# Kernel tuning notes

Measured on AMD Instinct MI355X. Metric: run time of the kernel, lower is better.

Reference implementation:

```python
import jax, jax.numpy as jnp
import numpy as np

DS = 32   # self_obs_dim
DO = 32   # obstacle_obs_dim
D = DS + DO
H = 128   # obstacle_hidden_size
B = 512   # batch_size
A = 16    # num_adv_obs = 2 * num_oppo_obs


def _init_linear(key, fan_in, fan_out):
    kw, kb = jax.random.split(key)
    bound = 1.0 / np.sqrt(fan_in)
    w = jax.random.uniform(kw, (fan_in, fan_out), jnp.float32, -bound, bound)
    b = jax.random.uniform(kb, (fan_out,), jnp.float32, -bound, bound)
    return w, b


def setup_inputs() -> dict:
    key = jax.random.key(0)
    ks = jax.random.split(key, 10)
    obs = jax.random.normal(ks[0], (B, DS), jnp.float32)
    latent = jax.random.normal(ks[1], (B, A, DO), jnp.float32)
    hw1, hb1 = _init_linear(ks[2], D, H)
    hw2, hb2 = _init_linear(ks[3], H, D * H)
    vw1, vb1 = _init_linear(ks[4], H, H)
    vw2, vb2 = _init_linear(ks[5], H, H)
    aw1, ab1 = _init_linear(ks[6], 2 * H, H)
    aw2, ab2 = _init_linear(ks[7], H, H)
    aw3, ab3 = _init_linear(ks[8], H, 1)
    return {
        "obs": obs, "obs_intention_latent": latent,
        "hw1": hw1, "hb1": hb1, "hw2": hw2, "hb2": hb2,
        "vw1": vw1, "vb1": vb1, "vw2": vw2, "vb2": vb2,
        "aw1": aw1, "ab1": ab1, "aw2": aw2, "ab2": ab2,
        "aw3": aw3, "ab3": ab3,
        "num_adv_obs": A, "batch_size": B, "num_groups": 1,
    }


def reference(obs, obs_intention_latent, hw1, hb1, hw2, hb2,
              vw1, vb1, vw2, vb2, aw1, ab1, aw2, ab2, aw3, ab3,
              num_adv_obs, batch_size, num_groups):
    relu = jax.nn.relu
    # flatten opponents (batch-major, matches torch .reshape)
    obs_obstacles = obs_intention_latent.reshape(-1, DO)          # [N, DO]
    # torch .repeat(num_adv_obs, 1) tiles the batch dim
    self_rep = jnp.tile(obs[:, :DS], (num_adv_obs, 1))            # [N, DS]
    mlp_input = jnp.concatenate([self_rep, obs_obstacles], axis=1)  # [N, D]
    # hypernet: per-sample weight [N, D, H]
    h = relu(mlp_input @ hw1 + hb1)
    w = relu(h @ hw2 + hb2).reshape(-1, D, H)
    # per-sample vector-matrix product + tanh
    emb = jnp.tanh(jnp.einsum("nd,ndh->nh", mlp_input, w))        # [N, H]
    # neighbor value MLP
    vals = relu(relu(emb @ vw1 + vb1) @ vw2 + vb2)                # [N, H]
    # attention: concat with per-batch mean embedding
    emb_mean = jnp.mean(emb.reshape(batch_size, -1, H), axis=1)   # [B, H]
    mean_rep = jnp.tile(emb_mean, (num_adv_obs, 1))               # [N, H]
    att_in = jnp.concatenate([emb, mean_rep], axis=1)             # [N, 2H]
    scores = relu(relu(att_in @ aw1 + ab1) @ aw2 + ab2) @ aw3 + ab3  # [N, 1]
    att = jax.nn.softmax(scores.reshape(batch_size, -1), axis=1).reshape(-1, 1)
    weighted = (att * vals).reshape(batch_size, -1, H)
    return jnp.sum(weighted, axis=1)                              # [B, H]
```

## Files before the change

### kernel.cpp

```cpp
#include <hip/hip_runtime.h>
#include <hip/hip_bf16.h>
#include <math.h>

#define BATCH 512
#define NADV  16
#define NROWS (BATCH*NADV)
#define DS    32
#define DO    32
#define DIM   64
#define HID   128
#define WCOLS (DIM*HID)
#define LSTR  136
#define PACK_BLOCKS 276

typedef _Float16 half8 __attribute__((ext_vector_type(8)));
typedef float floatx4 __attribute__((ext_vector_type(4)));

__device__ inline void async_ld16(void* lds, const void* g) {
    __builtin_amdgcn_global_load_lds(
        (const __attribute__((address_space(1))) void*)g,
        (__attribute__((address_space(3))) void*)lds, 16, 0, 0);
}

__global__ __launch_bounds__(256)
void k_prep(const float* __restrict__ obs, const float* __restrict__ latent,
            const float* __restrict__ hw1, const float* __restrict__ hb1,
            const float* __restrict__ hw2, const float* __restrict__ vw1,
            const float* __restrict__ vw2, const float* __restrict__ aw1,
            const float* __restrict__ aw2,
            _Float16* __restrict__ hf,
            _Float16* __restrict__ w2p, _Float16* __restrict__ vw1p,
            _Float16* __restrict__ vw2p, _Float16* __restrict__ aw1p,
            _Float16* __restrict__ aw2p) {
    __shared__ __align__(16) float smem[32 * 132];
    int b = blockIdx.x;
    int tid = threadIdx.x;
    if (b < PACK_BLOCKS) {
        const float* src; _Float16* dst; int N, Kt, jb, kt;
        if (b < 256)      { src = hw2; dst = w2p;  N = WCOLS; Kt = 4; jb = b >> 2; kt = b & 3; }
        else if (b < 260) { src = vw1; dst = vw1p; N = HID;   Kt = 4; jb = 0; kt = b - 256; }
        else if (b < 264) { src = vw2; dst = vw2p; N = HID;   Kt = 4; jb = 0; kt = b - 260; }
        else if (b < 272) { src = aw1; dst = aw1p; N = HID;   Kt = 8; jb = 0; kt = b - 264; }
        else              { src = aw2; dst = aw2p; N = HID;   Kt = 4; jb = 0; kt = b - 272; }
        for (int i = tid; i < 32 * 32; i += 256) {
            int r = i >> 5, c4 = (i & 31) * 4;
            *(float4*)&smem[r * 132 + c4] =
                *(const float4*)(src + (size_t)(kt * 32 + r) * N + jb * 128 + c4);
        }
        __syncthreads();
        for (int i = tid; i < 8 * 64; i += 256) {
            int ctl = i >> 6, lane = i & 63;
            int ct = jb * 8 + ctl;
            int rbase = (lane >> 4) * 8, cc = ctl * 16 + (lane & 15);
            half8 v;
#pragma unroll
            for (int e = 0; e < 8; ++e) v[e] = (_Float16)smem[(rbase + e) * 132 + cc];
            *(half8*)(dst + ((size_t)ct * Kt + kt) * 512 + lane * 8) = v;
        }
    } else {
        int n0 = (b - PACK_BLOCKS) * 16;
        int wave = tid >> 6, lane = tid & 63, l15 = lane & 15, quad = lane >> 4;
        half8 af2[2];
        {
            int n = n0 + l15;
            const float* orow = obs + (size_t)(n & (BATCH - 1)) * DS + quad * 8;
            const float* lrow = latent + (size_t)n * DO + quad * 8;
            float4 a0 = *(const float4*)orow;
            float4 a1 = *(const float4*)(orow + 4);
            float4 c0 = *(const float4*)lrow;
            float4 c1 = *(const float4*)(lrow + 4);
            float a8[8] = {a0.x, a0.y, a0.z, a0.w, a1.x, a1.y, a1.z, a1.w};
            float c8[8] = {c0.x, c0.y, c0.z, c0.w, c1.x, c1.y, c1.z, c1.w};
#pragma unroll
            for (int e = 0; e < 8; ++e) {
                af2[0][e] = (_Float16)a8[e];
                af2[1][e] = (_Float16)c8[e];
            }
        }
#pragma unroll
        for (int cti = 0; cti < 2; ++cti) {
            int ct = wave * 2 + cti;
            float bb = hb1[ct * 16 + l15];
            floatx4 acc = {bb, bb, bb, bb};
#pragma unroll
            for (int ks = 0; ks < 2; ++ks) {
                const float* wsrc = hw1 + (size_t)(ks * 32 + quad * 8) * HID + ct * 16 + l15;
                half8 bf;
#pragma unroll
                for (int e = 0; e < 8; ++e) bf[e] = (_Float16)wsrc[e * HID];
                acc = __builtin_amdgcn_mfma_f32_16x16x32_f16(af2[ks], bf, acc, 0, 0, 0);
            }
#pragma unroll
            for (int reg = 0; reg < 4; ++reg)
                hf[(size_t)(n0 + quad * 4 + reg) * HID + ct * 16 + l15] =
                    (_Float16)fmaxf(acc[reg], 0.f);
        }
    }
}

__global__ __launch_bounds__(256, 2)
void k_hyper_mfma(const float* __restrict__ obs, const float* __restrict__ latent,
                  const _Float16* __restrict__ hf, const _Float16* __restrict__ w2p,
                  const float* __restrict__ hb2,
                  _Float16* __restrict__ embf, _Float16* __restrict__ emeanf) {
    __shared__ __align__(16) _Float16 Bs[8][4][512];
    __shared__ __align__(16) float xs_t[64][132];
    __shared__ float bias_s[64 * 16];
    int b  = blockIdx.x;
    int jt = b & 7;
    int rt = b >> 3;
    int n0 = rt * 128;
    int j0 = jt * 16;
    int tid = threadIdx.x;
    int wave = tid >> 6, lane = tid & 63;
    int l15 = lane & 15, quad = lane >> 4;

    for (int i = tid; i < 128 * 16; i += 256) {
        int r = i >> 4, c4 = (i & 15) * 4;
        float4 v;
        if (c4 < DS) v = *(const float4*)(obs + ((n0 + r) & (BATCH - 1)) * DS + c4);
        else         v = *(const float4*)(latent + (size_t)(n0 + r) * DO + (c4 - DS));
        xs_t[c4 + 0][r] = v.x;
        xs_t[c4 + 1][r] = v.y;
        xs_t[c4 + 2][r] = v.z;
        xs_t[c4 + 3][r] = v.w;
    }
    for (int i = tid; i < 64 * 16; i += 256)
        bias_s[i] = hb2[(i >> 4) * HID + j0 + (i & 15)];

    half8 af[2][4];
#pragma unroll
    for (int t = 0; t < 2; ++t) {
        const _Float16* arow = hf + (size_t)(n0 + wave * 32 + t * 16 + l15) * HID;
#pragma unroll
        for (int ks = 0; ks < 4; ++ks)
            af[t][ks] = *(const half8*)(arow + ks * 32 + quad * 8);
    }

    float emb_acc[2][4] = {{0.f, 0.f, 0.f, 0.f}, {0.f, 0.f, 0.f, 0.f}};

    for (int d8 = 0; d8 < 8; ++d8) {
#pragma unroll
        for (int s = 0; s < 2; ++s) {
            int dt = wave * 2 + s;
            int ct = (d8 * 8 + dt) * 8 + jt;
            const _Float16* src = w2p + (size_t)ct * 2048 + lane * 8;
            _Float16* dst = &Bs[dt][0][0];
#pragma unroll
            for (int kt = 0; kt < 4; ++kt)
                async_ld16(dst + kt * 512, src + kt * 512);
        }
        __syncthreads();

#pragma unroll
        for (int dd = 0; dd < 8; ++dd) {
            int d = d8 * 8 + dd;
            float bb = bias_s[d * 16 + l15];
            floatx4 acc0 = {bb, bb, bb, bb};
            floatx4 acc1 = {bb, bb, bb, bb};
#pragma unroll
            for (int ks = 0; ks < 4; ++ks) {
                half8 bfr = *(const half8*)&Bs[dd][ks][lane * 8];
                acc0 = __builtin_amdgcn_mfma_f32_16x16x32_f16(af[0][ks], bfr, acc0, 0, 0, 0);
                acc1 = __builtin_amdgcn_mfma_f32_16x16x32_f16(af[1][ks], bfr, acc1, 0, 0, 0);
            }
            floatx4 xv0 = *(const floatx4*)&xs_t[d][wave * 32 + quad * 4];
            floatx4 xv1 = *(const floatx4*)&xs_t[d][wave * 32 + 16 + quad * 4];
#pragma unroll
            for (int reg = 0; reg < 4; ++reg) {
                emb_acc[0][reg] = fmaf(xv0[reg], fmaxf(acc0[reg], 0.f), emb_acc[0][reg]);
                emb_acc[1][reg] = fmaf(xv1[reg], fmaxf(acc1[reg], 0.f), emb_acc[1][reg]);
            }
        }
        __syncthreads();
    }

#pragma unroll
    for (int t = 0; t < 2; ++t) {
        float e[4];
#pragma unroll
        for (int reg = 0; reg < 4; ++reg) {
            e[reg] = tanhf(emb_acc[t][reg]);
            embf[(size_t)(n0 + wave * 32 + t * 16 + quad * 4 + reg) * HID + j0 + l15] =
                (_Float16)e[reg];
        }
        float s = e[0] + e[1] + e[2] + e[3];
        s += __shfl_xor(s, 16, 64);
        s += __shfl_xor(s, 32, 64);
        if (quad == 0)
            emeanf[(size_t)(rt * 8 + wave * 2 + t) * HID + j0 + l15] =
                (_Float16)(s * (1.f / 16));
    }
}

__global__ __launch_bounds__(512, 4)
void k_tail(const _Float16* __restrict__ embf, const _Float16* __restrict__ emeanf,
            const _Float16* __restrict__ vw1p, const float* __restrict__ vb1,
            const _Float16* __restrict__ vw2p, const float* __restrict__ vb2,
            const _Float16* __restrict__ aw1p, const float* __restrict__ ab1,
            const _Float16* __restrict__ aw2p, const float* __restrict__ ab2,
            const float* __restrict__ aw3, const float* __restrict__ ab3,
            float* __restrict__ out) {
    __shared__ _Float16 embs[16][LSTR];
    __shared__ _Float16 means[16][LSTR];
    __shared__ _Float16 tAs[16][LSTR];
    __shared__ _Float16 tBs[16][LSTR];
    __shared__ float scr[16][32];
    __shared__ float satt[16];
    __shared__ float att[16];
    int g = blockIdx.x;
    int n0 = g * 16;
    int tid = threadIdx.x;
    int wave = tid >> 6, lane = tid & 63, l15 = lane & 15, quad = lane >> 4;
    int ct = wave;

    {
        int m = tid >> 8, r = (tid >> 4) & 15, c8 = (tid & 15) * 8;
        if (m == 0)
            *(half8*)&embs[r][c8] = *(const half8*)(embf + (size_t)(n0 + r) * HID + c8);
        else
            *(half8*)&means[r][c8] =
                *(const half8*)(emeanf + (size_t)((n0 & 511) + r) * HID + c8);
    }
    __syncthreads();

    half8 av[4], amean[4];
#pragma unroll
    for (int ks = 0; ks < 4; ++ks) {
        av[ks]    = *(const half8*)&embs[l15][ks * 32 + quad * 8];
        amean[ks] = *(const half8*)&means[l15][ks * 32 + quad * 8];
    }

    floatx4 acc;
    {
        float bb = vb1[ct * 16 + l15];
        acc = (floatx4){bb, bb, bb, bb};
    }
#pragma unroll
    for (int ks = 0; ks < 4; ++ks) {
        half8 bfr = *(const half8*)(vw1p + ((size_t)ct * 4 + ks) * 512 + lane * 8);
        acc = __builtin_amdgcn_mfma_f32_16x16x32_f16(av[ks], bfr, acc, 0, 0, 0);
    }
#pragma unroll
    for (int reg = 0; reg < 4; ++reg)
        tAs[quad * 4 + reg][ct * 16 + l15] = (_Float16)fmaxf(acc[reg], 0.f);
    __syncthreads();

    half8 at[4];
#pragma unroll
    for (int ks = 0; ks < 4; ++ks)
        at[ks] = *(const half8*)&tAs[l15][ks * 32 + quad * 8];

    floatx4 vacc;
    {
        float bb = vb2[ct * 16 + l15];
        vacc = (floatx4){bb, bb, bb, bb};
    }
#pragma unroll
    for (int ks = 0; ks < 4; ++ks) {
        half8 bfr = *(const half8*)(vw2p + ((size_t)ct * 4 + ks) * 512 + lane * 8);
        vacc = __builtin_amdgcn_mfma_f32_16x16x32_f16(at[ks], bfr, vacc, 0, 0, 0);
    }

    floatx4 aacc;
    {
        float bb = ab1[ct * 16 + l15];
        aacc = (floatx4){bb, bb, bb, bb};
    }
#pragma unroll
    for (int ks = 0; ks < 8; ++ks) {
        half8 bfr = *(const half8*)(aw1p + ((size_t)ct * 8 + ks) * 512 + lane * 8);
        half8 a = (ks < 4) ? av[ks] : amean[ks - 4];
        aacc = __builtin_amdgcn_mfma_f32_16x16x32_f16(a, bfr, aacc, 0, 0, 0);
    }
#pragma unroll
    for (int reg = 0; reg < 4; ++reg)
        tBs[quad * 4 + reg][ct * 16 + l15] = (_Float16)fmaxf(aacc[reg], 0.f);
    __syncthreads();

    half8 aa[4];
#pragma unroll
    for (int ks = 0; ks < 4; ++ks)
        aa[ks] = *(const half8*)&tBs[l15][ks * 32 + quad * 8];

    floatx4 a2acc;
    {
        float bb = ab2[ct * 16 + l15];
        a2acc = (floatx4){bb, bb, bb, bb};
    }
#pragma unroll
    for (int ks = 0; ks < 4; ++ks) {
        half8 bfr = *(const half8*)(aw2p + ((size_t)ct * 4 + ks) * 512 + lane * 8);
        a2acc = __builtin_amdgcn_mfma_f32_16x16x32_f16(aa[ks], bfr, a2acc, 0, 0, 0);
    }
    __syncthreads();
#pragma unroll
    for (int reg = 0; reg < 4; ++reg)
        tAs[quad * 4 + reg][ct * 16 + l15] = (_Float16)fmaxf(a2acc[reg], 0.f);
    __syncthreads();

    {
        int r = tid >> 5, ch = tid & 31;
        float p = 0.f;
#pragma unroll
        for (int k = 0; k < 4; ++k)
            p += (float)tAs[r][ch * 4 + k] * aw3[ch * 4 + k];
        scr[r][ch] = p;
    }
    __syncthreads();
    if (tid < 16) {
        float s = ab3[0];
#pragma unroll
        for (int ch = 0; ch < 32; ++ch) s += scr[tid][ch];
        satt[tid] = s;
    }
    __syncthreads();
    if (tid < 16) {
        float m = -1e30f;
#pragma unroll
        for (int a = 0; a < 16; ++a) m = fmaxf(m, satt[a]);
        float S = 0.f;
#pragma unroll
        for (int a = 0; a < 16; ++a) S += expf(satt[a] - m);
        att[tid] = expf(satt[tid] - m) / S;
    }
    __syncthreads();

    {
        float p = 0.f;
#pragma unroll
        for (int reg = 0; reg < 4; ++reg)
            p += att[quad * 4 + reg] * fmaxf(vacc[reg], 0.f);
        p += __shfl_xor(p, 16, 64);
        p += __shfl_xor(p, 32, 64);
        if (quad == 0) out[(size_t)g * HID + ct * 16 + l15] = p;
    }
}

extern "C" void kernel_launch(void* const* d_in, const int* in_sizes, int n_in,
                              void* d_out, int out_size, void* d_ws, size_t ws_size,
                              hipStream_t stream) {
    const float* obs = (const float*)d_in[0];
    const float* lat = (const float*)d_in[1];
    const float* hw1 = (const float*)d_in[2];
    const float* hb1 = (const float*)d_in[3];
    const float* hw2 = (const float*)d_in[4];
    const float* hb2 = (const float*)d_in[5];
    const float* vw1 = (const float*)d_in[6];
    const float* vb1 = (const float*)d_in[7];
    const float* vw2 = (const float*)d_in[8];
    const float* vb2 = (const float*)d_in[9];
    const float* aw1 = (const float*)d_in[10];
    const float* ab1 = (const float*)d_in[11];
    const float* aw2 = (const float*)d_in[12];
    const float* ab2 = (const float*)d_in[13];
    const float* aw3 = (const float*)d_in[14];
    const float* ab3 = (const float*)d_in[15];
    float* out = (float*)d_out;

    char* ws = (char*)d_ws;
    _Float16*  hf     = (_Float16*)ws;  ws += (size_t)NROWS * HID * 2;
    _Float16*  w2p    = (_Float16*)ws;  ws += (size_t)WCOLS * HID * 2;
    _Float16*  embf   = (_Float16*)ws;  ws += (size_t)NROWS * HID * 2;
    _Float16*  emeanf = (_Float16*)ws;  ws += (size_t)BATCH * HID * 2;
    _Float16*  vw1p   = (_Float16*)ws;  ws += (size_t)HID * HID * 2;
    _Float16*  vw2p   = (_Float16*)ws;  ws += (size_t)HID * HID * 2;
    _Float16*  aw1p   = (_Float16*)ws;  ws += (size_t)2 * HID * HID * 2;
    _Float16*  aw2p   = (_Float16*)ws;  ws += (size_t)HID * HID * 2;

    hipLaunchKernelGGL(k_prep, dim3(PACK_BLOCKS + NROWS / 16), dim3(256), 0, stream,
                       obs, lat, hw1, hb1, hw2, vw1, vw2, aw1, aw2,
                       hf, w2p, vw1p, vw2p, aw1p, aw2p);
    hipLaunchKernelGGL(k_hyper_mfma, dim3(512), dim3(256), 0, stream,
                       obs, lat, hf, w2p, hb2, embf, emeanf);
    hipLaunchKernelGGL(k_tail, dim3(BATCH), dim3(512), 0, stream,
                       embf, emeanf, vw1p, vb1, vw2p, vb2,
                       aw1p, ab1, aw2p, ab2, aw3, ab3, out);
}
```

Baseline: 128.0 us.

## Fuse three kernels into one persistent kernel with grid barriers

After: 223.0 us. +74.2%, slower.

```diff
diff --git a/kernel.cpp b/kernel.cpp
--- a/kernel.cpp
+++ b/kernel.cpp
@@ -12,6 +12,7 @@
 #define WCOLS (DIM*HID)
 #define LSTR  136
 #define PACK_BLOCKS 276
+#define NBLK  512
 
 typedef _Float16 half8 __attribute__((ext_vector_type(8)));
 typedef float floatx4 __attribute__((ext_vector_type(4)));
@@ -22,318 +23,338 @@
         (__attribute__((address_space(3))) void*)lds, 16, 0, 0);
 }
 
-__global__ __launch_bounds__(256)
-void k_prep(const float* __restrict__ obs, const float* __restrict__ latent,
-            const float* __restrict__ hw1, const float* __restrict__ hb1,
-            const float* __restrict__ hw2, const float* __restrict__ vw1,
-            const float* __restrict__ vw2, const float* __restrict__ aw1,
-            const float* __restrict__ aw2,
-            _Float16* __restrict__ hf,
-            _Float16* __restrict__ w2p, _Float16* __restrict__ vw1p,
-            _Float16* __restrict__ vw2p, _Float16* __restrict__ aw1p,
-            _Float16* __restrict__ aw2p) {
-    __shared__ __align__(16) float smem[32 * 132];
-    int b = blockIdx.x;
-    int tid = threadIdx.x;
-    if (b < PACK_BLOCKS) {
-        const float* src; _Float16* dst; int N, Kt, jb, kt;
-        if (b < 256)      { src = hw2; dst = w2p;  N = WCOLS; Kt = 4; jb = b >> 2; kt = b & 3; }
-        else if (b < 260) { src = vw1; dst = vw1p; N = HID;   Kt = 4; jb = 0; kt = b - 256; }
-        else if (b < 264) { src = vw2; dst = vw2p; N = HID;   Kt = 4; jb = 0; kt = b - 260; }
-        else if (b < 272) { src = aw1; dst = aw1p; N = HID;   Kt = 8; jb = 0; kt = b - 264; }
-        else              { src = aw2; dst = aw2p; N = HID;   Kt = 4; jb = 0; kt = b - 272; }
-        for (int i = tid; i < 32 * 32; i += 256) {
-            int r = i >> 5, c4 = (i & 31) * 4;
-            *(float4*)&smem[r * 132 + c4] =
-                *(const float4*)(src + (size_t)(kt * 32 + r) * N + jb * 128 + c4);
-        }
-        __syncthreads();
-        for (int i = tid; i < 8 * 64; i += 256) {
-            int ctl = i >> 6, lane = i & 63;
-            int ct = jb * 8 + ctl;
-            int rbase = (lane >> 4) * 8, cc = ctl * 16 + (lane & 15);
-            half8 v;
-#pragma unroll
-            for (int e = 0; e < 8; ++e) v[e] = (_Float16)smem[(rbase + e) * 132 + cc];
-            *(half8*)(dst + ((size_t)ct * Kt + kt) * 512 + lane * 8) = v;
-        }
-    } else {
-        int n0 = (b - PACK_BLOCKS) * 16;
-        int wave = tid >> 6, lane = tid & 63, l15 = lane & 15, quad = lane >> 4;
-        half8 af2[2];
-        {
-            int n = n0 + l15;
-            const float* orow = obs + (size_t)(n & (BATCH - 1)) * DS + quad * 8;
-            const float* lrow = latent + (size_t)n * DO + quad * 8;
-            float4 a0 = *(const float4*)orow;
-            float4 a1 = *(const float4*)(orow + 4);
-            float4 c0 = *(const float4*)lrow;
-            float4 c1 = *(const float4*)(lrow + 4);
-            float a8[8] = {a0.x, a0.y, a0.z, a0.w, a1.x, a1.y, a1.z, a1.w};
-            float c8[8] = {c0.x, c0.y, c0.z, c0.w, c1.x, c1.y, c1.z, c1.w};
-#pragma unroll
-            for (int e = 0; e < 8; ++e) {
-                af2[0][e] = (_Float16)a8[e];
-                af2[1][e] = (_Float16)c8[e];
-            }
-        }
-#pragma unroll
-        for (int cti = 0; cti < 2; ++cti) {
-            int ct = wave * 2 + cti;
-            float bb = hb1[ct * 16 + l15];
-            floatx4 acc = {bb, bb, bb, bb};
-#pragma unroll
-            for (int ks = 0; ks < 2; ++ks) {
-                const float* wsrc = hw1 + (size_t)(ks * 32 + quad * 8) * HID + ct * 16 + l15;
-                half8 bf;
-#pragma unroll
-                for (int e = 0; e < 8; ++e) bf[e] = (_Float16)wsrc[e * HID];
-                acc = __builtin_amdgcn_mfma_f32_16x16x32_f16(af2[ks], bf, acc, 0, 0, 0);
-            }
-#pragma unroll
-            for (int reg = 0; reg < 4; ++reg)
-                hf[(size_t)(n0 + quad * 4 + reg) * HID + ct * 16 + l15] =
-                    (_Float16)fmaxf(acc[reg], 0.f);
-        }
+__device__ inline void grid_barrier(unsigned* cnt) {
+    __syncthreads();
+    if (threadIdx.x == 0) {
+        __threadfence();
+        atomicAdd(cnt, 1u);
+        while (__hip_atomic_load(cnt, __ATOMIC_RELAXED,
+                                 __HIP_MEMORY_SCOPE_AGENT) < NBLK)
+            __builtin_amdgcn_s_sleep(2);
+        __threadfence();
     }
+    __syncthreads();
 }
 
 __global__ __launch_bounds__(256, 2)
-void k_hyper_mfma(const float* __restrict__ obs, const float* __restrict__ latent,
-                  const _Float16* __restrict__ hf, const _Float16* __restrict__ w2p,
-                  const float* __restrict__ hb2,
-                  _Float16* __restrict__ embf, _Float16* __restrict__ emeanf) {
-    __shared__ __align__(16) _Float16 Bs[8][4][512];
-    __shared__ __align__(16) float xs_t[64][132];
-    __shared__ float bias_s[64 * 16];
-    int b  = blockIdx.x;
-    int jt = b & 7;
-    int rt = b >> 3;
-    int n0 = rt * 128;
-    int j0 = jt * 16;
-    int tid = threadIdx.x;
-    int wave = tid >> 6, lane = tid & 63;
-    int l15 = lane & 15, quad = lane >> 4;
-
-    for (int i = tid; i < 128 * 16; i += 256) {
-        int r = i >> 4, c4 = (i & 15) * 4;
-        float4 v;
-        if (c4 < DS) v = *(const float4*)(obs + ((n0 + r) & (BATCH - 1)) * DS + c4);
-        else         v = *(const float4*)(latent + (size_t)(n0 + r) * DO + (c4 - DS));
-        xs_t[c4 + 0][r] = v.x;
-        xs_t[c4 + 1][r] = v.y;
-        xs_t[c4 + 2][r] = v.z;
-        xs_t[c4 + 3][r] = v.w;
-    }
-    for (int i = tid; i < 64 * 16; i += 256)
-        bias_s[i] = hb2[(i >> 4) * HID + j0 + (i & 15)];
-
-    half8 af[2][4];
-#pragma unroll
-    for (int t = 0; t < 2; ++t) {
-        const _Float16* arow = hf + (size_t)(n0 + wave * 32 + t * 16 + l15) * HID;
-#pragma unroll
-        for (int ks = 0; ks < 4; ++ks)
-            af[t][ks] = *(const half8*)(arow + ks * 32 + quad * 8);
-    }
-
-    float emb_acc[2][4] = {{0.f, 0.f, 0.f, 0.f}, {0.f, 0.f, 0.f, 0.f}};
-
-    for (int d8 = 0; d8 < 8; ++d8) {
-#pragma unroll
-        for (int s = 0; s < 2; ++s) {
-            int dt = wave * 2 + s;
-            int ct = (d8 * 8 + dt) * 8 + jt;
-            const _Float16* src = w2p + (size_t)ct * 2048 + lane * 8;
-            _Float16* dst = &Bs[dt][0][0];
-#pragma unroll
-            for (int kt = 0; kt < 4; ++kt)
-                async_ld16(dst + kt * 512, src + kt * 512);
-        }
-        __syncthreads();
-
-#pragma unroll
-        for (int dd = 0; dd < 8; ++dd) {
-            int d = d8 * 8 + dd;
-            float bb = bias_s[d * 16 + l15];
-            floatx4 acc0 = {bb, bb, bb, bb};
-            floatx4 acc1 = {bb, bb, bb, bb};
-#pragma unroll
-            for (int ks = 0; ks < 4; ++ks) {
-                half8 bfr = *(const half8*)&Bs[dd][ks][lane * 8];
-                acc0 = __builtin_amdgcn_mfma_f32_16x16x32_f16(af[0][ks], bfr, acc0, 0, 0, 0);
-                acc1 = __builtin_amdgcn_mfma_f32_16x16x32_f16(af[1][ks], bfr, acc1, 0, 0, 0);
-            }
-            floatx4 xv0 = *(const floatx4*)&xs_t[d][wave * 32 + quad * 4];
-            floatx4 xv1 = *(const floatx4*)&xs_t[d][wave * 32 + 16 + quad * 4];
-#pragma unroll
-            for (int reg = 0; reg < 4; ++reg) {
-                emb_acc[0][reg] = fmaf(xv0[reg], fmaxf(acc0[reg], 0.f), emb_acc[0][reg]);
-                emb_acc[1][reg] = fmaf(xv1[reg], fmaxf(acc1[reg], 0.f), emb_acc[1][reg]);
-            }
-        }
-        __syncthreads();
-    }
-
-#pragma unroll
-    for (int t = 0; t < 2; ++t) {
-        float e[4];
-#pragma unroll
-        for (int reg = 0; reg < 4; ++reg) {
-            e[reg] = tanhf(emb_acc[t][reg]);
-            embf[(size_t)(n0 + wave * 32 + t * 16 + quad * 4 + reg) * HID + j0 + l15] =
-                (_Float16)e[reg];
-        }
-        float s = e[0] + e[1] + e[2] + e[3];
-        s += __shfl_xor(s, 16, 64);
-        s += __shfl_xor(s, 32, 64);
-        if (quad == 0)
-            emeanf[(size_t)(rt * 8 + wave * 2 + t) * HID + j0 + l15] =
-                (_Float16)(s * (1.f / 16));
-    }
-}
-
-__global__ __launch_bounds__(512, 4)
-void k_tail(const _Float16* __restrict__ embf, const _Float16* __restrict__ emeanf,
-            const _Float16* __restrict__ vw1p, const float* __restrict__ vb1,
-            const _Float16* __restrict__ vw2p, const float* __restrict__ vb2,
-            const _Float16* __restrict__ aw1p, const float* __restrict__ ab1,
-            const _Float16* __restrict__ aw2p, const float* __restrict__ ab2,
-            const float* __restrict__ aw3, const float* __restrict__ ab3,
-            float* __restrict__ out) {
-    __shared__ _Float16 embs[16][LSTR];
-    __shared__ _Float16 means[16][LSTR];
-    __shared__ _Float16 tAs[16][LSTR];
-    __shared__ _Float16 tBs[16][LSTR];
-    __shared__ float scr[16][32];
-    __shared__ float satt[16];
-    __shared__ float att[16];
-    int g = blockIdx.x;
-    int n0 = g * 16;
+void k_fused(const float* __restrict__ obs, const float* __restrict__ latent,
+             const float* __restrict__ hw1, const float* __restrict__ hb1,
+             const float* __restrict__ hw2, const float* __restrict__ hb2,
+             const float* __restrict__ vw1, const float* __restrict__ vb1,
+             const float* __restrict__ vw2, const float* __restrict__ vb2,
+             const float* __restrict__ aw1, const float* __restrict__ ab1,
+             const float* __restrict__ aw2, const float* __restrict__ ab2,
+             const float* __restrict__ aw3, const float* __restrict__ ab3,
+             float* __restrict__ out,
+             _Float16* __restrict__ hf, _Float16* __restrict__ w2p,
+             _Float16* __restrict__ embf, _Float16* __restrict__ emeanf,
+             _Float16* __restrict__ vw1p, _Float16* __restrict__ vw2p,
+             _Float16* __restrict__ aw1p, _Float16* __restrict__ aw2p,
+             unsigned* __restrict__ bar) {
+    __shared__ __align__(16) char smraw[70656];
+    int b   = blockIdx.x;
     int tid = threadIdx.x;
     int wave = tid >> 6, lane = tid & 63, l15 = lane & 15, quad = lane >> 4;
-    int ct = wave;
 
     {
-        int m = tid >> 8, r = (tid >> 4) & 15, c8 = (tid & 15) * 8;
-        if (m == 0)
-            *(half8*)&embs[r][c8] = *(const half8*)(embf + (size_t)(n0 + r) * HID + c8);
-        else
-            *(half8*)&means[r][c8] =
-                *(const half8*)(emeanf + (size_t)((n0 & 511) + r) * HID + c8);
+        float* smem = (float*)smraw;
+        if (b < PACK_BLOCKS) {
+            const float* src; _Float16* dst; int N, Kt, jb, kt;
+            if (b < 256)      { src = hw2; dst = w2p;  N = WCOLS; Kt = 4; jb = b >> 2; kt = b & 3; }
+            else if (b < 260) { src = vw1; dst = vw1p; N = HID;   Kt = 4; jb = 0; kt = b - 256; }
+            else if (b < 264) { src = vw2; dst = vw2p; N = HID;   Kt = 4; jb = 0; kt = b - 260; }
+            else if (b < 272) { src = aw1; dst = aw1p; N = HID;   Kt = 8; jb = 0; kt = b - 264; }
+            else              { src = aw2; dst = aw2p; N = HID;   Kt = 4; jb = 0; kt = b - 272; }
+            for (int i = tid; i < 32 * 32; i += 256) {
+                int r = i >> 5, c4 = (i & 31) * 4;
+                *(float4*)&smem[r * 132 + c4] =
+                    *(const float4*)(src + (size_t)(kt * 32 + r) * N + jb * 128 + c4);
+            }
+            __syncthreads();
+            for (int i = tid; i < 8 * 64; i += 256) {
+                int ctl = i >> 6, ln = i & 63;
+                int ct = jb * 8 + ctl;
+                int rbase = (ln >> 4) * 8, cc = ctl * 16 + (ln & 15);
+                half8 v;
+#pragma unroll
+                for (int e = 0; e < 8; ++e) v[e] = (_Float16)smem[(rbase + e) * 132 + cc];
+                *(half8*)(dst + ((size_t)ct * Kt + kt) * 512 + ln * 8) = v;
+            }
+        }
+        int hgroup = (b < PACK_BLOCKS) ? (b + NBLK - PACK_BLOCKS) : (b - PACK_BLOCKS);
+        {
+            int n0 = hgroup * 16;
+            half8 af2[2];
+            {
+                int n = n0 + l15;
+                const float* orow = obs + (size_t)(n & (BATCH - 1)) * DS + quad * 8;
+                const float* lrow = latent + (size_t)n * DO + quad * 8;
+                float4 a0 = *(const float4*)orow;
+                float4 a1 = *(const float4*)(orow + 4);
+                float4 c0 = *(const float4*)lrow;
+                float4 c1 = *(const float4*)(lrow + 4);
+                float a8[8] = {a0.x, a0.y, a0.z, a0.w, a1.x, a1.y, a1.z, a1.w};
+                float c8[8] = {c0.x, c0.y, c0.z, c0.w, c1.x, c1.y, c1.z, c1.w};
+#pragma unroll
+                for (int e = 0; e < 8; ++e) {
+                    af2[0][e] = (_Float16)a8[e];
+                    af2[1][e] = (_Float16)c8[e];
+                }
+            }
+#pragma unroll
+            for (int cti = 0; cti < 2; ++cti) {
+                int ct = wave * 2 + cti;
+                float bb = hb1[ct * 16 + l15];
+                floatx4 acc = {bb, bb, bb, bb};
+#pragma unroll
+                for (int ks = 0; ks < 2; ++ks) {
+                    const float* wsrc = hw1 + (size_t)(ks * 32 + quad * 8) * HID + ct * 16 + l15;
+                    half8 bf;
+#pragma unroll
+                    for (int e = 0; e < 8; ++e) bf[e] = (_Float16)wsrc[e * HID];
+                    acc = __builtin_amdgcn_mfma_f32_16x16x32_f16(af2[ks], bf, acc, 0, 0, 0);
+                }
+#pragma unroll
+                for (int reg = 0; reg < 4; ++reg)
+                    hf[(size_t)(n0 + quad * 4 + reg) * HID + ct * 16 + l15] =
+                        (_Float16)fmaxf(acc[reg], 0.f);
+            }
+        }
     }
-    __syncthreads();
-
-    half8 av[4], amean[4];
-#pragma unroll
-    for (int ks = 0; ks < 4; ++ks) {
-        av[ks]    = *(const half8*)&embs[l15][ks * 32 + quad * 8];
-        amean[ks] = *(const half8*)&means[l15][ks * 32 + quad * 8];
+    grid_barrier(bar + 0);
+
+    {
+        _Float16 (*Bs)[4][512] = (_Float16(*)[4][512])smraw;
+        float (*xs_t)[132]     = (float(*)[132])(smraw + 32768);
+        float* bias_s          = (float*)(smraw + 66560);
+        int jt = b & 7;
+        int rt = b >> 3;
+        int n0 = rt * 128;
+        int j0 = jt * 16;
+
+        for (int i = tid; i < 128 * 16; i += 256) {
+            int r = i >> 4, c4 = (i & 15) * 4;
+            float4 v;
+            if (c4 < DS) v = *(const float4*)(obs + ((n0 + r) & (BATCH - 1)) * DS + c4);
+            else         v = *(const float4*)(latent + (size_t)(n0 + r) * DO + (c4 - DS));
+            xs_t[c4 + 0][r] = v.x;
+            xs_t[c4 + 1][r] = v.y;
+            xs_t[c4 + 2][r] = v.z;
+            xs_t[c4 + 3][r] = v.w;
+        }
+        for (int i = tid; i < 64 * 16; i += 256)
+            bias_s[i] = hb2[(i >> 4) * HID + j0 + (i & 15)];
+
+        half8 af[2][4];
+#pragma unroll
+        for (int t = 0; t < 2; ++t) {
+            const _Float16* arow = hf + (size_t)(n0 + wave * 32 + t * 16 + l15) * HID;
+#pragma unroll
+            for (int ks = 0; ks < 4; ++ks)
+                af[t][ks] = *(const half8*)(arow + ks * 32 + quad * 8);
+        }
+
+        float emb_acc[2][4] = {{0.f, 0.f, 0.f, 0.f}, {0.f, 0.f, 0.f, 0.f}};
+
+        for (int d8 = 0; d8 < 8; ++d8) {
+#pragma unroll
+            for (int s = 0; s < 2; ++s) {
+                int dt = wave * 2 + s;
+                int ct = (d8 * 8 + dt) * 8 + jt;
+                const _Float16* src = w2p + (size_t)ct * 2048 + lane * 8;
+                _Float16* dst = &Bs[dt][0][0];
+#pragma unroll
+                for (int kt = 0; kt < 4; ++kt)
+                    async_ld16(dst + kt * 512, src + kt * 512);
+            }
+            __syncthreads();
+
+#pragma unroll
+            for (int dd = 0; dd < 8; ++dd) {
+                int d = d8 * 8 + dd;
+                float bb = bias_s[d * 16 + l15];
+                floatx4 acc0 = {bb, bb, bb, bb};
+                floatx4 acc1 = {bb, bb, bb, bb};
+#pragma unroll
+                for (int ks = 0; ks < 4; ++ks) {
+                    half8 bfr = *(const half8*)&Bs[dd][ks][lane * 8];
+                    acc0 = __builtin_amdgcn_mfma_f32_16x16x32_f16(af[0][ks], bfr, acc0, 0, 0, 0);
+                    acc1 = __builtin_amdgcn_mfma_f32_16x16x32_f16(af[1][ks], bfr, acc1, 0, 0, 0);
+                }
+                floatx4 xv0 = *(const floatx4*)&xs_t[d][wave * 32 + quad * 4];
+                floatx4 xv1 = *(const floatx4*)&xs_t[d][wave * 32 + 16 + quad * 4];
+#pragma unroll
+                for (int reg = 0; reg < 4; ++reg) {
+                    emb_acc[0][reg] = fmaf(xv0[reg], fmaxf(acc0[reg], 0.f), emb_acc[0][reg]);
+                    emb_acc[1][reg] = fmaf(xv1[reg], fmaxf(acc1[reg], 0.f), emb_acc[1][reg]);
+                }
+            }
+            __syncthreads();
+        }
+
+#pragma unroll
+        for (int t = 0; t < 2; ++t) {
+            float e[4];
+#pragma unroll
+            for (int reg = 0; reg < 4; ++reg) {
+                e[reg] = tanhf(emb_acc[t][reg]);
+                embf[(size_t)(n0 + wave * 32 + t * 16 + quad * 4 + reg) * HID + j0 + l15] =
+                    (_Float16)e[reg];
+            }
+            float s = e[0] + e[1] + e[2] + e[3];
+            s += __shfl_xor(s, 16, 64);
+            s += __shfl_xor(s, 32, 64);
+            if (quad == 0)
+                emeanf[(size_t)(rt * 8 + wave * 2 + t) * HID + j0 + l15] =
+                    (_Float16)(s * (1.f / 16));
+        }
     }
-
-    floatx4 acc;
+    grid_barrier(bar + 64);
+
     {
-        float bb = vb1[ct * 16 + l15];
-        acc = (floatx4){bb, bb, bb, bb};
-    }
-#pragma unroll
-    for (int ks = 0; ks < 4; ++ks) {
-        half8 bfr = *(const half8*)(vw1p + ((size_t)ct * 4 + ks) * 512 + lane * 8);
-        acc = __builtin_amdgcn_mfma_f32_16x16x32_f16(av[ks], bfr, acc, 0, 0, 0);
-    }
-#pragma unroll
-    for (int reg = 0; reg < 4; ++reg)
-        tAs[quad * 4 + reg][ct * 16 + l15] = (_Float16)fmaxf(acc[reg], 0.f);
-    __syncthreads();
-
-    half8 at[4];
-#pragma unroll
-    for (int ks = 0; ks < 4; ++ks)
-        at[ks] = *(const half8*)&tAs[l15][ks * 32 + quad * 8];
-
-    floatx4 vacc;
-    {
-        float bb = vb2[ct * 16 + l15];
-        vacc = (floatx4){bb, bb, bb, bb};
-    }
-#pragma unroll
-    for (int ks = 0; ks < 4; ++ks) {
-        half8 bfr = *(const half8*)(vw2p + ((size_t)ct * 4 + ks) * 512 + lane * 8);
-        vacc = __builtin_amdgcn_mfma_f32_16x16x32_f16(at[ks], bfr, vacc, 0, 0, 0);
-    }
-
-    floatx4 aacc;
-    {
-        float bb = ab1[ct * 16 + l15];
-        aacc = (floatx4){bb, bb, bb, bb};
-    }
-#pragma unroll
-    for (int ks = 0; ks < 8; ++ks) {
-        half8 bfr = *(const half8*)(aw1p + ((size_t)ct * 8 + ks) * 512 + lane * 8);
-        half8 a = (ks < 4) ? av[ks] : amean[ks - 4];
-        aacc = __builtin_amdgcn_mfma_f32_16x16x32_f16(a, bfr, aacc, 0, 0, 0);
-    }
-#pragma unroll
-    for (int reg = 0; reg < 4; ++reg)
-        tBs[quad * 4 + reg][ct * 16 + l15] = (_Float16)fmaxf(aacc[reg], 0.f);
-    __syncthreads();
-
-    half8 aa[4];
-#pragma unroll
-    for (int ks = 0; ks < 4; ++ks)
-        aa[ks] = *(const half8*)&tBs[l15][ks * 32 + quad * 8];
-
-    floatx4 a2acc;
-    {
-        float bb = ab2[ct * 16 + l15];
-        a2acc = (floatx4){bb, bb, bb, bb};
-    }
-#pragma unroll
-    for (int ks = 0; ks < 4; ++ks) {
-        half8 bfr = *(const half8*)(aw2p + ((size_t)ct * 4 + ks) * 512 + lane * 8);
-        a2acc = __builtin_amdgcn_mfma_f32_16x16x32_f16(aa[ks], bfr, a2acc, 0, 0, 0);
-    }
-    __syncthreads();
-#pragma unroll
-    for (int reg = 0; reg < 4; ++reg)
-        tAs[quad * 4 + reg][ct * 16 + l15] = (_Float16)fmaxf(a2acc[reg], 0.f);
-    __syncthreads();
-
-    {
-        int r = tid >> 5, ch = tid & 31;
-        float p = 0.f;
-#pragma unroll
-        for (int k = 0; k < 4; ++k)
-            p += (float)tAs[r][ch * 4 + k] * aw3[ch * 4 + k];
-        scr[r][ch] = p;
-    }
-    __syncthreads();
-    if (tid < 16) {
-        float s = ab3[0];
-#pragma unroll
-        for (int ch = 0; ch < 32; ++ch) s += scr[tid][ch];
-        satt[tid] = s;
-    }
-    __syncthreads();
-    if (tid < 16) {
-        float m = -1e30f;
-#pragma unroll
-        for (int a = 0; a < 16; ++a) m = fmaxf(m, satt[a]);
-        float S = 0.f;
-#pragma unroll
-        for (int a = 0; a < 16; ++a) S += expf(satt[a] - m);
-        att[tid] = expf(satt[tid] - m) / S;
-    }
-    __syncthreads();
-
-    {
-        float p = 0.f;
-#pragma unroll
-        for (int reg = 0; reg < 4; ++reg)
-            p += att[quad * 4 + reg] * fmaxf(vacc[reg], 0.f);
-        p += __shfl_xor(p, 16, 64);
-        p += __shfl_xor(p, 32, 64);
-        if (quad == 0) out[(size_t)g * HID + ct * 16 + l15] = p;
+        _Float16 (*embs)[LSTR]  = (_Float16(*)[LSTR])smraw;
+        _Float16 (*means)[LSTR] = (_Float16(*)[LSTR])(smraw + 4352);
+        _Float16 (*tAs)[LSTR]   = (_Float16(*)[LSTR])(smraw + 8704);
+        _Float16 (*tBs)[LSTR]   = (_Float16(*)[LSTR])(smraw + 13056);
+        float (*scr)[16]        = (float(*)[16])(smraw + 17408);
+        float* satt             = (float*)(smraw + 18432);
+        float* att              = (float*)(smraw + 18496);
+        int g = b;
+        int n0 = g * 16;
+
+        for (int i = tid; i < 512; i += 256) {
+            int m = i >> 8, r = (i >> 4) & 15, c8 = (i & 15) * 8;
+            if (m == 0)
+                *(half8*)&embs[r][c8] = *(const half8*)(embf + (size_t)(n0 + r) * HID + c8);
+            else
+                *(half8*)&means[r][c8] =
+                    *(const half8*)(emeanf + (size_t)((n0 + r) & 511) * HID + c8);
+        }
+        __syncthreads();
+
+        half8 av[4], amean[4];
+#pragma unroll
+        for (int ks = 0; ks < 4; ++ks) {
+            av[ks]    = *(const half8*)&embs[l15][ks * 32 + quad * 8];
+            amean[ks] = *(const half8*)&means[l15][ks * 32 + quad * 8];
+        }
+
+#pragma unroll
+        for (int cti = 0; cti < 2; ++cti) {
+            int ct = wave + cti * 4;
+            float bb = vb1[ct * 16 + l15];
+            floatx4 acc = {bb, bb, bb, bb};
+#pragma unroll
+            for (int ks = 0; ks < 4; ++ks) {
+                half8 bfr = *(const half8*)(vw1p + ((size_t)ct * 4 + ks) * 512 + lane * 8);
+                acc = __builtin_amdgcn_mfma_f32_16x16x32_f16(av[ks], bfr, acc, 0, 0, 0);
+            }
+#pragma unroll
+            for (int reg = 0; reg < 4; ++reg)
+                tAs[quad * 4 + reg][ct * 16 + l15] = (_Float16)fmaxf(acc[reg], 0.f);
+        }
+        __syncthreads();
+
+        half8 at4[4];
+#pragma unroll
+        for (int ks = 0; ks < 4; ++ks)
+            at4[ks] = *(const half8*)&tAs[l15][ks * 32 + quad * 8];
+
+        floatx4 vacc[2];
+#pragma unroll
+        for (int cti = 0; cti < 2; ++cti) {
+            int ct = wave + cti * 4;
+            float bb = vb2[ct * 16 + l15];
+            vacc[cti] = (floatx4){bb, bb, bb, bb};
+#pragma unroll
+            for (int ks = 0; ks < 4; ++ks) {
+                half8 bfr = *(const half8*)(vw2p + ((size_t)ct * 4 + ks) * 512 + lane * 8);
+                vacc[cti] = __builtin_amdgcn_mfma_f32_16x16x32_f16(at4[ks], bfr, vacc[cti], 0, 0, 0);
+            }
+        }
+
+#pragma unroll
+        for (int cti = 0; cti < 2; ++cti) {
+            int ct = wave + cti * 4;
+            float bb = ab1[ct * 16 + l15];
+            floatx4 aacc = {bb, bb, bb, bb};
+#pragma unroll
+            for (int ks = 0; ks < 8; ++ks) {
+                half8 bfr = *(const half8*)(aw1p + ((size_t)ct * 8 + ks) * 512 + lane * 8);
+                half8 a = (ks < 4) ? av[ks] : amean[ks - 4];
+                aacc = __builtin_amdgcn_mfma_f32_16x16x32_f16(a, bfr, aacc, 0, 0, 0);
+            }
+#pragma unroll
+            for (int reg = 0; reg < 4; ++reg)
+                tBs[quad * 4 + reg][ct * 16 + l15] = (_Float16)fmaxf(aacc[reg], 0.f);
+        }
+        __syncthreads();
+
+        half8 aa[4];
+#pragma unroll
+        for (int ks = 0; ks < 4; ++ks)
+            aa[ks] = *(const half8*)&tBs[l15][ks * 32 + quad * 8];
+
+        floatx4 a2acc[2];
+#pragma unroll
+        for (int cti = 0; cti < 2; ++cti) {
+            int ct = wave + cti * 4;
+            float bb = ab2[ct * 16 + l15];
+            a2acc[cti] = (floatx4){bb, bb, bb, bb};
+#pragma unroll
+            for (int ks = 0; ks < 4; ++ks) {
+                half8 bfr = *(const half8*)(aw2p + ((size_t)ct * 4 + ks) * 512 + lane * 8);
+                a2acc[cti] = __builtin_amdgcn_mfma_f32_16x16x32_f16(aa[ks], bfr, a2acc[cti], 0, 0, 0);
+            }
+        }
+        __syncthreads();
+#pragma unroll
+        for (int cti = 0; cti < 2; ++cti) {
+            int ct = wave + cti * 4;
+#pragma unroll
+            for (int reg = 0; reg < 4; ++reg)
+                tAs[quad * 4 + reg][ct * 16 + l15] = (_Float16)fmaxf(a2acc[cti][reg], 0.f);
+        }
+        __syncthreads();
+
+        {
+            int r = tid >> 4, ch = tid & 15;
+            float p = 0.f;
+#pragma unroll
+            for (int k = 0; k < 8; ++k)
+                p += (float)tAs[r][ch * 8 + k] * aw3[ch * 8 + k];
+            scr[r][ch] = p;
+        }
+        __syncthreads();
+        if (tid < 16) {
+            float s = ab3[0];
+#pragma unroll
+            for (int ch = 0; ch < 16; ++ch) s += scr[tid][ch];
+            satt[tid] = s;
+        }
+        __syncthreads();
+        if (tid < 16) {
+            float m = -1e30f;
+#pragma unroll
+            for (int a = 0; a < 16; ++a) m = fmaxf(m, satt[a]);
+            float S = 0.f;
+#pragma unroll
+            for (int a = 0; a < 16; ++a) S += expf(satt[a] - m);
+            att[tid] = expf(satt[tid] - m) / S;
+        }
+        __syncthreads();
+
+#pragma unroll
+        for (int cti = 0; cti < 2; ++cti) {
+            int ct = wave + cti * 4;
+            float p = 0.f;
+#pragma unroll
+            for (int reg = 0; reg < 4; ++reg)
+                p += att[quad * 4 + reg] * fmaxf(vacc[cti][reg], 0.f);
+            p += __shfl_xor(p, 16, 64);
+            p += __shfl_xor(p, 32, 64);
+            if (quad == 0) out[(size_t)g * HID + ct * 16 + l15] = p;
+        }
     }
 }
 
@@ -367,13 +388,11 @@
     _Float16*  vw2p   = (_Float16*)ws;  ws += (size_t)HID * HID * 2;
     _Float16*  aw1p   = (_Float16*)ws;  ws += (size_t)2 * HID * HID * 2;
     _Float16*  aw2p   = (_Float16*)ws;  ws += (size_t)HID * HID * 2;
-
-    hipLaunchKernelGGL(k_prep, dim3(PACK_BLOCKS + NROWS / 16), dim3(256), 0, stream,
-                       obs, lat, hw1, hb1, hw2, vw1, vw2, aw1, aw2,
-                       hf, w2p, vw1p, vw2p, aw1p, aw2p);
-    hipLaunchKernelGGL(k_hyper_mfma, dim3(512), dim3(256), 0, stream,
-                       obs, lat, hf, w2p, hb2, embf, emeanf);
-    hipLaunchKernelGGL(k_tail, dim3(BATCH), dim3(512), 0, stream,
-                       embf, emeanf, vw1p, vb1, vw2p, vb2,
-                       aw1p, ab1, aw2p, ab2, aw3, ab3, out);
+    unsigned* bar = (unsigned*)((char*)d_ws + (8u << 20));
+    hipMemsetAsync(bar, 0, 512, stream);
+
+    hipLaunchKernelGGL(k_fused, dim3(NBLK), dim3(256), 0, stream,
+                       obs, lat, hw1, hb1, hw2, hb2, vw1, vb1, vw2, vb2,
+                       aw1, ab1, aw2, ab2, aw3, ab3, out,
+                       hf, w2p, embf, emeanf, vw1p, vw2p, aw1p, aw2p, bar);
 }
```

## Fuse prep into hypernet kernel, convert hw2 on the fly with register prefetch

Applied to the files above, without the earlier changes.

Measured after the change: 138.1 us. 1.08x slower.

```diff
diff --git a/kernel.cpp b/kernel.cpp
--- a/kernel.cpp
+++ b/kernel.cpp
@@ -11,109 +11,58 @@
 #define HID   128
 #define WCOLS (DIM*HID)
 #define LSTR  136
-#define PACK_BLOCKS 276
 
 typedef _Float16 half8 __attribute__((ext_vector_type(8)));
 typedef float floatx4 __attribute__((ext_vector_type(4)));
 
-__device__ inline void async_ld16(void* lds, const void* g) {
-    __builtin_amdgcn_global_load_lds(
-        (const __attribute__((address_space(1))) void*)g,
-        (__attribute__((address_space(3))) void*)lds, 16, 0, 0);
-}
-
-__global__ __launch_bounds__(256)
-void k_prep(const float* __restrict__ obs, const float* __restrict__ latent,
+__global__ __launch_bounds__(256, 2)
+void k_main(const float* __restrict__ obs, const float* __restrict__ latent,
             const float* __restrict__ hw1, const float* __restrict__ hb1,
-            const float* __restrict__ hw2, const float* __restrict__ vw1,
-            const float* __restrict__ vw2, const float* __restrict__ aw1,
-            const float* __restrict__ aw2,
-            _Float16* __restrict__ hf,
-            _Float16* __restrict__ w2p, _Float16* __restrict__ vw1p,
-            _Float16* __restrict__ vw2p, _Float16* __restrict__ aw1p,
-            _Float16* __restrict__ aw2p) {
-    __shared__ __align__(16) float smem[32 * 132];
-    int b = blockIdx.x;
+            const float* __restrict__ hw2, const float* __restrict__ hb2,
+            const float* __restrict__ vw1, const float* __restrict__ vw2,
+            const float* __restrict__ aw1, const float* __restrict__ aw2,
+            _Float16* __restrict__ embf, _Float16* __restrict__ emeanf,
+            _Float16* __restrict__ vw1p, _Float16* __restrict__ vw2p,
+            _Float16* __restrict__ aw1p, _Float16* __restrict__ aw2p) {
+    __shared__ __align__(16) char smraw[71680];
+    int b   = blockIdx.x;
     int tid = threadIdx.x;
-    if (b < PACK_BLOCKS) {
-        const float* src; _Float16* dst; int N, Kt, jb, kt;
-        if (b < 256)      { src = hw2; dst = w2p;  N = WCOLS; Kt = 4; jb = b >> 2; kt = b & 3; }
-        else if (b < 260) { src = vw1; dst = vw1p; N = HID;   Kt = 4; jb = 0; kt = b - 256; }
-        else if (b < 264) { src = vw2; dst = vw2p; N = HID;   Kt = 4; jb = 0; kt = b - 260; }
-        else if (b < 272) { src = aw1; dst = aw1p; N = HID;   Kt = 8; jb = 0; kt = b - 264; }
-        else              { src = aw2; dst = aw2p; N = HID;   Kt = 4; jb = 0; kt = b - 272; }
+    int wave = tid >> 6, lane = tid & 63, l15 = lane & 15, quad = lane >> 4;
+
+    if (b >= 512) {
+        float* smem = (float*)smraw;
+        int u = b - 512;
+        const float* src; _Float16* dst; int Kt, kt;
+        if (u < 4)       { src = vw1; dst = vw1p; Kt = 4; kt = u; }
+        else if (u < 8)  { src = vw2; dst = vw2p; Kt = 4; kt = u - 4; }
+        else if (u < 16) { src = aw1; dst = aw1p; Kt = 8; kt = u - 8; }
+        else             { src = aw2; dst = aw2p; Kt = 4; kt = u - 16; }
         for (int i = tid; i < 32 * 32; i += 256) {
             int r = i >> 5, c4 = (i & 31) * 4;
             *(float4*)&smem[r * 132 + c4] =
-                *(const float4*)(src + (size_t)(kt * 32 + r) * N + jb * 128 + c4);
+                *(const float4*)(src + (size_t)(kt * 32 + r) * HID + c4);
         }
         __syncthreads();
         for (int i = tid; i < 8 * 64; i += 256) {
-            int ctl = i >> 6, lane = i & 63;
-            int ct = jb * 8 + ctl;
-            int rbase = (lane >> 4) * 8, cc = ctl * 16 + (lane & 15);
+            int ctl = i >> 6, ln = i & 63;
+            int rbase = (ln >> 4) * 8, cc = ctl * 16 + (ln & 15);
             half8 v;
 #pragma unroll
             for (int e = 0; e < 8; ++e) v[e] = (_Float16)smem[(rbase + e) * 132 + cc];
-            *(half8*)(dst + ((size_t)ct * Kt + kt) * 512 + lane * 8) = v;
-        }
-    } else {
-        int n0 = (b - PACK_BLOCKS) * 16;
-        int wave = tid >> 6, lane = tid & 63, l15 = lane & 15, quad = lane >> 4;
-        half8 af2[2];
-        {
-            int n = n0 + l15;
-            const float* orow = obs + (size_t)(n & (BATCH - 1)) * DS + quad * 8;
-            const float* lrow = latent + (size_t)n * DO + quad * 8;
-            float4 a0 = *(const float4*)orow;
-            float4 a1 = *(const float4*)(orow + 4);
-            float4 c0 = *(const float4*)lrow;
-            float4 c1 = *(const float4*)(lrow + 4);
-            float a8[8] = {a0.x, a0.y, a0.z, a0.w, a1.x, a1.y, a1.z, a1.w};
-            float c8[8] = {c0.x, c0.y, c0.z, c0.w, c1.x, c1.y, c1.z, c1.w};
-#pragma unroll
-            for (int e = 0; e < 8; ++e) {
-                af2[0][e] = (_Float16)a8[e];
-                af2[1][e] = (_Float16)c8[e];
-            }
-        }
-#pragma unroll
-        for (int cti = 0; cti < 2; ++cti) {
-            int ct = wave * 2 + cti;
-            float bb = hb1[ct * 16 + l15];
-            floatx4 acc = {bb, bb, bb, bb};
-#pragma unroll
-            for (int ks = 0; ks < 2; ++ks) {
-                const float* wsrc = hw1 + (size_t)(ks * 32 + quad * 8) * HID + ct * 16 + l15;
-                half8 bf;
-#pragma unroll
-                for (int e = 0; e < 8; ++e) bf[e] = (_Float16)wsrc[e * HID];
-                acc = __builtin_amdgcn_mfma_f32_16x16x32_f16(af2[ks], bf, acc, 0, 0, 0);
-            }
-#pragma unroll
-            for (int reg = 0; reg < 4; ++reg)
-                hf[(size_t)(n0 + quad * 4 + reg) * HID + ct * 16 + l15] =
-                    (_Float16)fmaxf(acc[reg], 0.f);
-        }
-    }
-}
-
-__global__ __launch_bounds__(256, 2)
-void k_hyper_mfma(const float* __restrict__ obs, const float* __restrict__ latent,
-                  const _Float16* __restrict__ hf, const _Float16* __restrict__ w2p,
-                  const float* __restrict__ hb2,
-                  _Float16* __restrict__ embf, _Float16* __restrict__ emeanf) {
-    __shared__ __align__(16) _Float16 Bs[8][4][512];
-    __shared__ __align__(16) float xs_t[64][132];
-    __shared__ float bias_s[64 * 16];
-    int b  = blockIdx.x;
+            *(half8*)(dst + ((size_t)ctl * Kt + kt) * 512 + ln * 8) = v;
+        }
+        return;
+    }
+
+    float (*xs_t)[132] = (float(*)[132])smraw;
+    _Float16* hscr_all = (_Float16*)(smraw + 33792);
+    _Float16 (*Bs)[2][4][512] = (_Float16(*)[2][4][512])(smraw + 33792);
+    float* bias_s = (float*)(smraw + 67584);
+
     int jt = b & 7;
     int rt = b >> 3;
     int n0 = rt * 128;
     int j0 = jt * 16;
-    int tid = threadIdx.x;
-    int wave = tid >> 6, lane = tid & 63;
-    int l15 = lane & 15, quad = lane >> 4;
 
     for (int i = tid; i < 128 * 16; i += 256) {
         int r = i >> 4, c4 = (i & 15) * 4;
@@ -128,39 +77,100 @@
     for (int i = tid; i < 64 * 16; i += 256)
         bias_s[i] = hb2[(i >> 4) * HID + j0 + (i & 15)];
 
+    _Float16* hscr = hscr_all + wave * (32 * 132);
     half8 af[2][4];
-#pragma unroll
-    for (int t = 0; t < 2; ++t) {
-        const _Float16* arow = hf + (size_t)(n0 + wave * 32 + t * 16 + l15) * HID;
-#pragma unroll
-        for (int ks = 0; ks < 4; ++ks)
-            af[t][ks] = *(const half8*)(arow + ks * 32 + quad * 8);
-    }
+    {
+        half8 afx[2][2];
+#pragma unroll
+        for (int t = 0; t < 2; ++t) {
+            int n = n0 + wave * 32 + t * 16 + l15;
+            const float* orow = obs + (size_t)(n & (BATCH - 1)) * DS + quad * 8;
+            const float* lrow = latent + (size_t)n * DO + quad * 8;
+#pragma unroll
+            for (int e = 0; e < 4; ++e) {
+                afx[t][0][e]     = (_Float16)orow[e];
+                afx[t][0][e + 4] = (_Float16)orow[e + 4];
+                afx[t][1][e]     = (_Float16)lrow[e];
+                afx[t][1][e + 4] = (_Float16)lrow[e + 4];
+            }
+        }
+#pragma unroll
+        for (int ct = 0; ct < 8; ++ct) {
+            half8 bf[2];
+#pragma unroll
+            for (int ks = 0; ks < 2; ++ks) {
+                const float* wsrc = hw1 + (size_t)(ks * 32 + quad * 8) * HID + ct * 16 + l15;
+#pragma unroll
+                for (int e = 0; e < 8; ++e) bf[ks][e] = (_Float16)wsrc[(size_t)e * HID];
+            }
+            float bb = hb1[ct * 16 + l15];
+#pragma unroll
+            for (int t = 0; t < 2; ++t) {
+                floatx4 acc = {bb, bb, bb, bb};
+#pragma unroll
+                for (int ks = 0; ks < 2; ++ks)
+                    acc = __builtin_amdgcn_mfma_f32_16x16x32_f16(afx[t][ks], bf[ks], acc, 0, 0, 0);
+#pragma unroll
+                for (int reg = 0; reg < 4; ++reg)
+                    hscr[(t * 16 + quad * 4 + reg) * 132 + ct * 16 + l15] =
+                        (_Float16)fmaxf(acc[reg], 0.f);
+            }
+        }
+#pragma unroll
+        for (int t = 0; t < 2; ++t)
+#pragma unroll
+            for (int ks = 0; ks < 4; ++ks)
+                af[t][ks] = *(const half8*)&hscr[(t * 16 + l15) * 132 + ks * 32 + quad * 8];
+    }
+    __syncthreads();
 
     float emb_acc[2][4] = {{0.f, 0.f, 0.f, 0.f}, {0.f, 0.f, 0.f, 0.f}};
 
-    for (int d8 = 0; d8 < 8; ++d8) {
-#pragma unroll
-        for (int s = 0; s < 2; ++s) {
-            int dt = wave * 2 + s;
-            int ct = (d8 * 8 + dt) * 8 + jt;
-            const _Float16* src = w2p + (size_t)ct * 2048 + lane * 8;
-            _Float16* dst = &Bs[dt][0][0];
-#pragma unroll
-            for (int kt = 0; kt < 4; ++kt)
-                async_ld16(dst + kt * 512, src + kt * 512);
-        }
-        __syncthreads();
-
-#pragma unroll
-        for (int dd = 0; dd < 8; ++dd) {
-            int d = d8 * 8 + dd;
+    {
+        float g[16];
+#pragma unroll
+        for (int ci = 0; ci < 2; ++ci) {
+            int c = wave * 2 + ci, dt = c >> 2, kt = c & 3;
+            const float* src = hw2 + (size_t)(kt * 32 + quad * 8) * WCOLS
+                                   + (size_t)dt * 128 + j0 + l15;
+#pragma unroll
+            for (int e = 0; e < 8; ++e) g[ci * 8 + e] = src[(size_t)e * WCOLS];
+        }
+#pragma unroll
+        for (int ci = 0; ci < 2; ++ci) {
+            int c = wave * 2 + ci, dt = c >> 2, kt = c & 3;
+            half8 v;
+#pragma unroll
+            for (int e = 0; e < 8; ++e) v[e] = (_Float16)g[ci * 8 + e];
+            *(half8*)&Bs[0][dt][kt][lane * 8] = v;
+        }
+    }
+    __syncthreads();
+
+    for (int it = 0; it < 32; ++it) {
+        int cb = it & 1;
+        bool have = (it < 31);
+        float g[16];
+        if (have) {
+#pragma unroll
+            for (int ci = 0; ci < 2; ++ci) {
+                int c = wave * 2 + ci, dt = c >> 2, kt = c & 3;
+                int d = (it + 1) * 2 + dt;
+                const float* src = hw2 + (size_t)(kt * 32 + quad * 8) * WCOLS
+                                       + (size_t)d * 128 + j0 + l15;
+#pragma unroll
+                for (int e = 0; e < 8; ++e) g[ci * 8 + e] = src[(size_t)e * WCOLS];
+            }
+        }
+#pragma unroll
+        for (int dd = 0; dd < 2; ++dd) {
+            int d = it * 2 + dd;
             float bb = bias_s[d * 16 + l15];
             floatx4 acc0 = {bb, bb, bb, bb};
             floatx4 acc1 = {bb, bb, bb, bb};
 #pragma unroll
             for (int ks = 0; ks < 4; ++ks) {
-                half8 bfr = *(const half8*)&Bs[dd][ks][lane * 8];
+                half8 bfr = *(const half8*)&Bs[cb][dd][ks][lane * 8];
                 acc0 = __builtin_amdgcn_mfma_f32_16x16x32_f16(af[0][ks], bfr, acc0, 0, 0, 0);
                 acc1 = __builtin_amdgcn_mfma_f32_16x16x32_f16(af[1][ks], bfr, acc1, 0, 0, 0);
             }
@@ -170,6 +180,16 @@
             for (int reg = 0; reg < 4; ++reg) {
                 emb_acc[0][reg] = fmaf(xv0[reg], fmaxf(acc0[reg], 0.f), emb_acc[0][reg]);
                 emb_acc[1][reg] = fmaf(xv1[reg], fmaxf(acc1[reg], 0.f), emb_acc[1][reg]);
+            }
+        }
+        if (have) {
+#pragma unroll
+            for (int ci = 0; ci < 2; ++ci) {
+                int c = wave * 2 + ci, dt = c >> 2, kt = c & 3;
+                half8 v;
+#pragma unroll
+                for (int e = 0; e < 8; ++e) v[e] = (_Float16)g[ci * 8 + e];
+                *(half8*)&Bs[cb ^ 1][dt][kt][lane * 8] = v;
             }
         }
         __syncthreads();
@@ -359,8 +379,6 @@
     float* out = (float*)d_out;
 
     char* ws = (char*)d_ws;
-    _Float16*  hf     = (_Float16*)ws;  ws += (size_t)NROWS * HID * 2;
-    _Float16*  w2p    = (_Float16*)ws;  ws += (size_t)WCOLS * HID * 2;
     _Float16*  embf   = (_Float16*)ws;  ws += (size_t)NROWS * HID * 2;
     _Float16*  emeanf = (_Float16*)ws;  ws += (size_t)BATCH * HID * 2;
     _Float16*  vw1p   = (_Float16*)ws;  ws += (size_t)HID * HID * 2;
@@ -368,11 +386,9 @@
     _Float16*  aw1p   = (_Float16*)ws;  ws += (size_t)2 * HID * HID * 2;
     _Float16*  aw2p   = (_Float16*)ws;  ws += (size_t)HID * HID * 2;
 
-    hipLaunchKernelGGL(k_prep, dim3(PACK_BLOCKS + NROWS / 16), dim3(256), 0, stream,
-                       obs, lat, hw1, hb1, hw2, vw1, vw2, aw1, aw2,
-                       hf, w2p, vw1p, vw2p, aw1p, aw2p);
-    hipLaunchKernelGGL(k_hyper_mfma, dim3(512), dim3(256), 0, stream,
-                       obs, lat, hf, w2p, hb2, embf, emeanf);
+    hipLaunchKernelGGL(k_main, dim3(532), dim3(256), 0, stream,
+                       obs, lat, hw1, hb1, hw2, hb2, vw1, vw2, aw1, aw2,
+                       embf, emeanf, vw1p, vw2p, aw1p, aw2p);
     hipLaunchKernelGGL(k_tail, dim3(BATCH), dim3(512), 0, stream,
                        embf, emeanf, vw1p, vb1, vw2p, vb2,
                        aw1p, ab1, aw2p, ab2, aw3, ab3, out);
```
